# Optimization experiments

Hardware: AMD Instinct MI355X
Metric: run time of the kernel (lower is better)

## Reference

```python
import jax, jax.numpy as jnp
import numpy as np

C = 256
DR = 32  # C // reduction

def setup_inputs() -> dict:
    key = jax.random.key(0)
    ks = jax.random.split(key, 8)
    B, H, W = 8, 64, 64
    x = jax.random.normal(ks[0], (B, C, H, W), dtype=jnp.float32)
    # 1x1 conv weights stored as [out, in] matrices + biases
    sq = 1.0 / np.sqrt(C)
    Wq = jax.random.uniform(ks[1], (DR, C), minval=-sq, maxval=sq, dtype=jnp.float32)
    bq = jax.random.uniform(ks[2], (DR,), minval=-sq, maxval=sq, dtype=jnp.float32)
    Wk = jax.random.uniform(ks[3], (DR, C), minval=-sq, maxval=sq, dtype=jnp.float32)
    bk = jax.random.uniform(ks[4], (DR,), minval=-sq, maxval=sq, dtype=jnp.float32)
    Wv = jax.random.uniform(ks[5], (C, C), minval=-sq, maxval=sq, dtype=jnp.float32)
    bv = jax.random.uniform(ks[6], (C,), minval=-sq, maxval=sq, dtype=jnp.float32)
    gamma = jnp.zeros((1,), dtype=jnp.float32) + 0.5  # nonzero so output depends on attention
    return {"x": x, "Wq": Wq, "bq": bq, "Wk": Wk, "bk": bk, "Wv": Wv, "bv": bv, "gamma": gamma}

def reference(x, Wq, bq, Wk, bk, Wv, bv, gamma):
    B, Cc, H, W = x.shape
    N = H * W
    xf = x.reshape(B, Cc, N)                                   # [B,C,N]
    q = jnp.einsum('dc,bcn->bdn', Wq, xf) + bq[None, :, None]  # [B,DR,N]
    k = jnp.einsum('dc,bcn->bdn', Wk, xf) + bk[None, :, None]  # [B,DR,N]
    v = jnp.einsum('ec,bcn->ben', Wv, xf) + bv[None, :, None]  # [B,C,N]
    attn = jnp.einsum('bdi,bdj->bij', q, k)                    # [B,N,N]
    attn = jax.nn.softmax(attn, axis=-1)
    out = jnp.einsum('bcj,bij->bci', v, attn)                  # [B,C,N]
    out = out.reshape(B, Cc, H, W)
    return gamma * out + x
```

## Files before the change

### kernel.cpp

```cpp
#include <hip/hip_runtime.h>

#define LOG2E 1.44269504088896340736f

typedef short v8s __attribute__((ext_vector_type(8)));
typedef float v4f __attribute__((ext_vector_type(4)));
typedef unsigned int v2u __attribute__((ext_vector_type(2)));

__device__ __forceinline__ unsigned short f2bf(float f) {
  unsigned int u = __float_as_uint(f);
  u += 0x7fffu + ((u >> 16) & 1u);
  return (unsigned short)(u >> 16);
}

__device__ __forceinline__ unsigned int cvtpk(float lo, float hi) {
  unsigned int r;
  asm("v_cvt_pk_bf16_f32 %0, %1, %2" : "=v"(r) : "v"(lo), "v"(hi));
  return r;
}

#define MFMA16(a, b, c) __builtin_amdgcn_mfma_f32_16x16x32_bf16((a), (b), (c), 0, 0, 0)

static const int CCH = 256, NPIX = 4096;

__global__ void wconv_kernel(const float* __restrict__ Wq, const float* __restrict__ Wk,
                             const float* __restrict__ Wv, unsigned short* __restrict__ wqk,
                             unsigned short* __restrict__ wvb) {
  int idx = blockIdx.x * 256 + threadIdx.x;
  int tot = 64 * 256 + 256 * 256;
  for (int i = idx; i < tot; i += gridDim.x * 256) {
    if (i < 64 * 256) {
      float v = (i < 32 * 256) ? Wq[i] : Wk[i - 32 * 256];
      wqk[i] = f2bf(v);
    } else {
      wvb[i - 64 * 256] = f2bf(Wv[i - 64 * 256]);
    }
  }
}

__global__ void xpose_kernel(const float* __restrict__ x, unsigned short* __restrict__ xT) {
  __shared__ float tile[64][65];
  int bid = blockIdx.x;
  int b = bid >> 8;
  int c0 = ((bid >> 6) & 3) * 64;
  int n0 = (bid & 63) * 64;
  int t = threadIdx.x;
  const float* xp = x + ((size_t)b * CCH + c0) * NPIX + n0;
#pragma unroll
  for (int p = 0; p < 16; ++p) {
    int cc = p * 4 + (t >> 6);
    int nn = t & 63;
    tile[cc][nn] = xp[(size_t)cc * NPIX + nn];
  }
  __syncthreads();
  unsigned short* xo = xT + ((size_t)b * NPIX + n0) * CCH + c0;
#pragma unroll
  for (int p = 0; p < 8; ++p) {
    int nn = p * 8 + (t >> 5);
    int cc = (t & 31) * 2;
    unsigned int pk = (unsigned int)f2bf(tile[cc][nn]) |
                      ((unsigned int)f2bf(tile[cc + 1][nn]) << 16);
    *(unsigned int*)(xo + (size_t)nn * CCH + cc) = pk;
  }
}

__global__ __launch_bounds__(256, 2) void qkproj_kernel(
    const unsigned short* __restrict__ xT, const unsigned short* __restrict__ wqk,
    const float* __restrict__ bq, const float* __restrict__ bk,
    unsigned short* __restrict__ qb, unsigned short* __restrict__ kb) {
  int bid = blockIdx.x;
  int b = bid >> 6;
  int n0 = (bid & 63) * 64;
  int w = threadIdx.x >> 6, lane = threadIdx.x & 63, g = lane >> 4, li = lane & 15;
  int nrow = n0 + 16 * w;
  v4f acc[4];
#pragma unroll
  for (int dt = 0; dt < 4; ++dt) acc[dt] = (v4f){0.f, 0.f, 0.f, 0.f};
#pragma unroll
  for (int ks = 0; ks < 8; ++ks) {
    v8s a = *(const v8s*)(xT + ((size_t)(b * NPIX + nrow + li)) * CCH + ks * 32 + g * 8);
#pragma unroll
    for (int dt = 0; dt < 4; ++dt) {
      v8s bf = *(const v8s*)(wqk + (dt * 16 + li) * 256 + ks * 32 + g * 8);
      acc[dt] = MFMA16(a, bf, acc[dt]);
    }
  }
#pragma unroll
  for (int dt = 0; dt < 4; ++dt) {
    int d = (dt & 1) * 16 + li;
    float bias = (dt < 2) ? bq[d] : bk[d];
    unsigned short* op = (dt < 2) ? qb : kb;
#pragma unroll
    for (int r = 0; r < 4; ++r) {
      int n = nrow + 4 * g + r;
      op[((size_t)(b * NPIX + n)) * 32 + d] = f2bf(acc[dt][r] + bias);
    }
  }
}

__global__ __launch_bounds__(256, 2) void vproj_kernel(
    const unsigned short* __restrict__ xT, const unsigned short* __restrict__ wvb,
    const float* __restrict__ bv, unsigned short* __restrict__ vb) {
  int bid = blockIdx.x;
  int b = bid >> 6;
  int n0 = (bid & 63) * 64;
  int w = threadIdx.x >> 6, lane = threadIdx.x & 63, g = lane >> 4, li = lane & 15;
  v4f acc[4][4];
#pragma unroll
  for (int ct = 0; ct < 4; ++ct)
#pragma unroll
    for (int nt = 0; nt < 4; ++nt) acc[ct][nt] = (v4f){0.f, 0.f, 0.f, 0.f};
#pragma unroll
  for (int ks = 0; ks < 8; ++ks) {
    v8s xf[4];
#pragma unroll
    for (int nt = 0; nt < 4; ++nt)
      xf[nt] = *(const v8s*)(xT + ((size_t)(b * NPIX + n0 + nt * 16 + li)) * CCH + ks * 32 + g * 8);
#pragma unroll
    for (int ct = 0; ct < 4; ++ct) {
      v8s wf = *(const v8s*)(wvb + (w * 64 + ct * 16 + li) * 256 + ks * 32 + g * 8);
#pragma unroll
      for (int nt = 0; nt < 4; ++nt) acc[ct][nt] = MFMA16(wf, xf[nt], acc[ct][nt]);
    }
  }
#pragma unroll
  for (int ct = 0; ct < 4; ++ct)
#pragma unroll
    for (int r = 0; r < 4; ++r) {
      int c = w * 64 + ct * 16 + 4 * g + r;
      float bias = bv[c];
#pragma unroll
      for (int nt = 0; nt < 4; ++nt) {
        int n = n0 + nt * 16 + li;
        vb[((size_t)(b * CCH + c)) * NPIX + n] = f2bf(acc[ct][nt][r] + bias);
      }
    }
}

#define PSWZ(il, jl) (((il) * 64 + (jl)) ^ (((il) & 7) << 3))
__global__ __launch_bounds__(512, 4) void attn_kernel(
    const unsigned short* __restrict__ qb, const unsigned short* __restrict__ kb,
    const unsigned short* __restrict__ vb, const float* __restrict__ x,
    const float* __restrict__ gamma, float* __restrict__ out) {
  __shared__ __align__(16) unsigned short pbuf[2][64 * 64];
  __shared__ float fbuf[2][64];
  __shared__ float lbuf[64];
  int bx = blockIdx.x;
  int wg = (bx & 7) * 64 + (bx >> 3);
  int b = wg >> 6, it = wg & 63;
  int i0 = it * 64;
  int w = threadIdx.x >> 6, lane = threadIdx.x & 63, g = lane >> 4, li = lane & 15;
  bool prod = (w < 4);

  float mraw = -1e30f, ml2 = -1.44e30f, ls = 0.f;
  v4f acc[2][4];
#pragma unroll
  for (int ct = 0; ct < 2; ++ct)
#pragma unroll
    for (int itl = 0; itl < 4; ++itl) acc[ct][itl] = (v4f){0.f, 0.f, 0.f, 0.f};
  const v4f vzero = {0.f, 0.f, 0.f, 0.f};

  const unsigned short* vb0 = vb + ((size_t)(b * CCH + w * 32 + li)) * NPIX + g * 8;
  const unsigned short* vbc[2];
#pragma unroll
  for (int ct = 0; ct < 2; ++ct) vbc[ct] = vb0 + (size_t)ct * 16 * NPIX;

  const unsigned short* kbase = kb + ((size_t)b * NPIX + li) * 32 + g * 8;
  v8s qf = {0, 0, 0, 0, 0, 0, 0, 0};
  v8s kf[4];
  if (prod) {
    qf = *(const v8s*)(qb + ((size_t)(b * NPIX + i0 + w * 16 + li)) * 32 + g * 8);
#pragma unroll
    for (int jt = 0; jt < 4; ++jt) kf[jt] = *(const v8s*)(kbase + (size_t)(jt * 16) * 32);
  }

  for (int jc = 0; jc < 64; ++jc) {
    int j0 = jc * 64, bsel = jc & 1;
    v8s vf[2][2];
#pragma unroll
    for (int ct = 0; ct < 2; ++ct)
#pragma unroll
      for (int sl = 0; sl < 2; ++sl)
        vf[ct][sl] = *(const v8s*)(vbc[ct] + j0 + sl * 32);
    if (prod) {
      __builtin_amdgcn_s_setprio(1);
      v4f s[4];
#pragma unroll
      for (int jt = 0; jt < 4; ++jt) s[jt] = MFMA16(kf[jt], qf, vzero);
      int jn = (jc < 63) ? j0 + 64 : j0;
#pragma unroll
      for (int jt = 0; jt < 4; ++jt)
        kf[jt] = *(const v8s*)(kbase + (size_t)(jn + jt * 16) * 32);
      float t0 = fmaxf(fmaxf(s[0][0], s[0][1]), fmaxf(s[0][2], s[0][3]));
      float t1 = fmaxf(fmaxf(s[1][0], s[1][1]), fmaxf(s[1][2], s[1][3]));
      float t2 = fmaxf(fmaxf(s[2][0], s[2][1]), fmaxf(s[2][2], s[2][3]));
      float t3 = fmaxf(fmaxf(s[3][0], s[3][1]), fmaxf(s[3][2], s[3][3]));
      float pmax = fmaxf(fmaxf(t0, t1), fmaxf(t2, t3));
      pmax = fmaxf(pmax, __shfl_xor(pmax, 16, 64));
      pmax = fmaxf(pmax, __shfl_xor(pmax, 32, 64));
      bool upd = pmax > mraw + 8.f;
      float nml2 = upd ? pmax * LOG2E : ml2;
      float fsc = __builtin_amdgcn_exp2f(ml2 - nml2);
      if (upd) { mraw = pmax; ml2 = nml2; }
      int il = w * 16 + li;
      float rs = 0.f;
#pragma unroll
      for (int jt = 0; jt < 4; ++jt) {
        float p0 = __builtin_amdgcn_exp2f(fmaf(s[jt][0], LOG2E, -nml2));
        float p1 = __builtin_amdgcn_exp2f(fmaf(s[jt][1], LOG2E, -nml2));
        float p2 = __builtin_amdgcn_exp2f(fmaf(s[jt][2], LOG2E, -nml2));
        float p3 = __builtin_amdgcn_exp2f(fmaf(s[jt][3], LOG2E, -nml2));
        rs += (p0 + p1) + (p2 + p3);
        v2u pk;
        pk.x = cvtpk(p0, p1);
        pk.y = cvtpk(p2, p3);
        *(v2u*)(&pbuf[bsel][PSWZ(il, jt * 16 + 4 * g)]) = pk;
      }
      rs += __shfl_xor(rs, 16, 64);
      rs += __shfl_xor(rs, 32, 64);
      ls = ls * fsc + rs;
      if (g == 0) fbuf[bsel][il] = fsc;
      asm volatile("s_waitcnt lgkmcnt(0)" ::: "memory");
      __builtin_amdgcn_s_setprio(0);
    }
    __builtin_amdgcn_s_barrier();
    asm volatile("" ::: "memory");
    float fv[4];
#pragma unroll
    for (int itl = 0; itl < 4; ++itl) fv[itl] = fbuf[bsel][itl * 16 + li];
    int anyr = (fv[0] != 1.f) | (fv[1] != 1.f) | (fv[2] != 1.f) | (fv[3] != 1.f);
    if (__any(anyr)) {
#pragma unroll
      for (int itl = 0; itl < 4; ++itl)
#pragma unroll
        for (int ct = 0; ct < 2; ++ct) acc[ct][itl] = acc[ct][itl] * fv[itl];
    }
#pragma unroll
    for (int itl = 0; itl < 4; ++itl) {
      v8s pf[2];
#pragma unroll
      for (int sl = 0; sl < 2; ++sl)
        pf[sl] = *(const v8s*)(&pbuf[bsel][PSWZ(itl * 16 + li, sl * 32 + g * 8)]);
#pragma unroll
      for (int ct = 0; ct < 2; ++ct)
#pragma unroll
        for (int sl = 0; sl < 2; ++sl) acc[ct][itl] = MFMA16(vf[ct][sl], pf[sl], acc[ct][itl]);
    }
  }
  if (prod && g == 0) lbuf[w * 16 + li] = ls;
  __syncthreads();
  float gm = gamma[0];
#pragma unroll
  for (int itl = 0; itl < 4; ++itl) {
    float inv = gm / lbuf[itl * 16 + li];
#pragma unroll
    for (int ct = 0; ct < 2; ++ct)
#pragma unroll
      for (int r = 0; r < 4; ++r) {
        int c = w * 32 + ct * 16 + 4 * g + r;
        size_t idx = ((size_t)(b * CCH + c)) * NPIX + i0 + itl * 16 + li;
        out[idx] = acc[ct][itl][r] * inv + x[idx];
      }
  }
}

extern "C" void kernel_launch(void* const* d_in, const int* in_sizes, int n_in,
                              void* d_out, int out_size, void* d_ws, size_t ws_size,
                              hipStream_t stream) {
  const float* x = (const float*)d_in[0];
  const float* Wq = (const float*)d_in[1];
  const float* bq = (const float*)d_in[2];
  const float* Wk = (const float*)d_in[3];
  const float* bk = (const float*)d_in[4];
  const float* Wv = (const float*)d_in[5];
  const float* bv = (const float*)d_in[6];
  const float* gamma = (const float*)d_in[7];
  float* out = (float*)d_out;
  char* ws = (char*)d_ws;
  unsigned short* xT  = (unsigned short*)(ws);
  unsigned short* qb  = (unsigned short*)(ws + 16777216);
  unsigned short* kb  = (unsigned short*)(ws + 18874368);
  unsigned short* vb  = (unsigned short*)(ws + 20971520);
  unsigned short* wqk = (unsigned short*)(ws + 37748736);
  unsigned short* wvb = (unsigned short*)(ws + 37781504);

  wconv_kernel<<<80, 256, 0, stream>>>(Wq, Wk, Wv, wqk, wvb);
  xpose_kernel<<<2048, 256, 0, stream>>>(x, xT);
  qkproj_kernel<<<512, 256, 0, stream>>>(xT, wqk, bq, bk, qb, kb);
  vproj_kernel<<<512, 256, 0, stream>>>(xT, wvb, bv, vb);
  attn_kernel<<<512, 512, 0, stream>>>(qb, kb, vb, x, gamma, out);
}
```

Measured before the change: 276.6 us.

## Software-pipeline softmax one chunk ahead of PV MFMAs in attention kernel

Adds a prologue that computes the first chunk's softmax probabilities before the loop, so each iteration computes the next chunk's QK scores and softmax into the other buffer while running the PV MFMAs on the current one. This overlaps the producer waves' softmax with their own PV work, which should cut the serialized barrier-to-barrier critical path. The conditional rescale skip is dropped, so rescaling now always runs, and the K prefetch moves two chunks ahead. Register pressure goes up because the score and PV state are live at the same time.

```diff
diff --git a/kernel.cpp b/kernel.cpp
--- a/kernel.cpp
+++ b/kernel.cpp
@@ -137,6 +137,52 @@
 }
 
 #define PSWZ(il, jl) (((il) * 64 + (jl)) ^ (((il) & 7) << 3))
+
+#define SOFTMAX_PUBLISH(PB)                                                    \
+  do {                                                                         \
+    float t0 = fmaxf(fmaxf(s[0][0], s[0][1]), fmaxf(s[0][2], s[0][3]));        \
+    float t1 = fmaxf(fmaxf(s[1][0], s[1][1]), fmaxf(s[1][2], s[1][3]));        \
+    float t2 = fmaxf(fmaxf(s[2][0], s[2][1]), fmaxf(s[2][2], s[2][3]));        \
+    float t3 = fmaxf(fmaxf(s[3][0], s[3][1]), fmaxf(s[3][2], s[3][3]));        \
+    float pmax = fmaxf(fmaxf(t0, t1), fmaxf(t2, t3));                          \
+    pmax = fmaxf(pmax, __shfl_xor(pmax, 16, 64));                              \
+    pmax = fmaxf(pmax, __shfl_xor(pmax, 32, 64));                              \
+    bool upd = pmax > mraw + 8.f;                                              \
+    float nml2 = upd ? pmax * LOG2E : ml2;                                     \
+    float fsc = __builtin_amdgcn_exp2f(ml2 - nml2);                            \
+    if (upd) { mraw = pmax; ml2 = nml2; }                                      \
+    float rs = 0.f;                                                            \
+    _Pragma("unroll")                                                          \
+    for (int jt = 0; jt < 4; ++jt) {                                           \
+      float p0 = __builtin_amdgcn_exp2f(fmaf(s[jt][0], LOG2E, -nml2));         \
+      float p1 = __builtin_amdgcn_exp2f(fmaf(s[jt][1], LOG2E, -nml2));         \
+      float p2 = __builtin_amdgcn_exp2f(fmaf(s[jt][2], LOG2E, -nml2));         \
+      float p3 = __builtin_amdgcn_exp2f(fmaf(s[jt][3], LOG2E, -nml2));         \
+      rs += (p0 + p1) + (p2 + p3);                                             \
+      v2u pk;                                                                  \
+      pk.x = cvtpk(p0, p1);                                                    \
+      pk.y = cvtpk(p2, p3);                                                    \
+      *(v2u*)(&pbuf[PB][PSWZ(il, jt * 16 + 4 * g)]) = pk;                      \
+    }                                                                          \
+    rs += __shfl_xor(rs, 16, 64);                                              \
+    rs += __shfl_xor(rs, 32, 64);                                              \
+    ls = ls * fsc + rs;                                                        \
+    if (g == 0) fbuf[PB][il] = fsc;                                            \
+  } while (0)
+
+#define PV_BLOCK                                                               \
+  do {                                                                         \
+    _Pragma("unroll")                                                          \
+    for (int itl = 0; itl < 4; ++itl) {                                        \
+      v8s pf0 = *(const v8s*)(&pbuf[bsel][PSWZ(itl * 16 + li, g * 8)]);        \
+      v8s pf1 = *(const v8s*)(&pbuf[bsel][PSWZ(itl * 16 + li, 32 + g * 8)]);   \
+      acc[0][itl] = MFMA16(vf[0][0], pf0, acc[0][itl]);                        \
+      acc[0][itl] = MFMA16(vf[0][1], pf1, acc[0][itl]);                        \
+      acc[1][itl] = MFMA16(vf[1][0], pf0, acc[1][itl]);                        \
+      acc[1][itl] = MFMA16(vf[1][1], pf1, acc[1][itl]);                        \
+    }                                                                          \
+  } while (0)
+
 __global__ __launch_bounds__(512, 4) void attn_kernel(
     const unsigned short* __restrict__ qb, const unsigned short* __restrict__ kb,
     const unsigned short* __restrict__ vb, const float* __restrict__ x,
@@ -150,6 +196,7 @@
   int i0 = it * 64;
   int w = threadIdx.x >> 6, lane = threadIdx.x & 63, g = lane >> 4, li = lane & 15;
   bool prod = (w < 4);
+  int il = w * 16 + li;
 
   float mraw = -1e30f, ml2 = -1.44e30f, ls = 0.f;
   v4f acc[2][4];
@@ -167,86 +214,58 @@
   const unsigned short* kbase = kb + ((size_t)b * NPIX + li) * 32 + g * 8;
   v8s qf = {0, 0, 0, 0, 0, 0, 0, 0};
   v8s kf[4];
+
   if (prod) {
     qf = *(const v8s*)(qb + ((size_t)(b * NPIX + i0 + w * 16 + li)) * 32 + g * 8);
 #pragma unroll
     for (int jt = 0; jt < 4; ++jt) kf[jt] = *(const v8s*)(kbase + (size_t)(jt * 16) * 32);
-  }
+    v4f s[4];
+#pragma unroll
+    for (int jt = 0; jt < 4; ++jt) s[jt] = MFMA16(kf[jt], qf, vzero);
+#pragma unroll
+    for (int jt = 0; jt < 4; ++jt)
+      kf[jt] = *(const v8s*)(kbase + (size_t)(64 + jt * 16) * 32);
+    SOFTMAX_PUBLISH(0);
+    asm volatile("s_waitcnt lgkmcnt(0)" ::: "memory");
+  }
+  __builtin_amdgcn_s_barrier();
+  asm volatile("" ::: "memory");
 
   for (int jc = 0; jc < 64; ++jc) {
-    int j0 = jc * 64, bsel = jc & 1;
+    int j0 = jc * 64, bsel = jc & 1, nb = bsel ^ 1;
     v8s vf[2][2];
 #pragma unroll
     for (int ct = 0; ct < 2; ++ct)
 #pragma unroll
       for (int sl = 0; sl < 2; ++sl)
         vf[ct][sl] = *(const v8s*)(vbc[ct] + j0 + sl * 32);
-    if (prod) {
+    float fv[4];
+#pragma unroll
+    for (int itl = 0; itl < 4; ++itl) fv[itl] = fbuf[bsel][itl * 16 + li];
+#pragma unroll
+    for (int itl = 0; itl < 4; ++itl)
+#pragma unroll
+      for (int ct = 0; ct < 2; ++ct) acc[ct][itl] = acc[ct][itl] * fv[itl];
+    if (prod && jc < 63) {
       __builtin_amdgcn_s_setprio(1);
       v4f s[4];
 #pragma unroll
       for (int jt = 0; jt < 4; ++jt) s[jt] = MFMA16(kf[jt], qf, vzero);
-      int jn = (jc < 63) ? j0 + 64 : j0;
+      int jn = (jc < 62) ? (jc + 2) * 64 : 4032;
 #pragma unroll
       for (int jt = 0; jt < 4; ++jt)
         kf[jt] = *(const v8s*)(kbase + (size_t)(jn + jt * 16) * 32);
-      float t0 = fmaxf(fmaxf(s[0][0], s[0][1]), fmaxf(s[0][2], s[0][3]));
-      float t1 = fmaxf(fmaxf(s[1][0], s[1][1]), fmaxf(s[1][2], s[1][3]));
-      float t2 = fmaxf(fmaxf(s[2][0], s[2][1]), fmaxf(s[2][2], s[2][3]));
-      float t3 = fmaxf(fmaxf(s[3][0], s[3][1]), fmaxf(s[3][2], s[3][3]));
-      float pmax = fmaxf(fmaxf(t0, t1), fmaxf(t2, t3));
-      pmax = fmaxf(pmax, __shfl_xor(pmax, 16, 64));
-      pmax = fmaxf(pmax, __shfl_xor(pmax, 32, 64));
-      bool upd = pmax > mraw + 8.f;
-      float nml2 = upd ? pmax * LOG2E : ml2;
-      float fsc = __builtin_amdgcn_exp2f(ml2 - nml2);
-      if (upd) { mraw = pmax; ml2 = nml2; }
-      int il = w * 16 + li;
-      float rs = 0.f;
-#pragma unroll
-      for (int jt = 0; jt < 4; ++jt) {
-        float p0 = __builtin_amdgcn_exp2f(fmaf(s[jt][0], LOG2E, -nml2));
-        float p1 = __builtin_amdgcn_exp2f(fmaf(s[jt][1], LOG2E, -nml2));
-        float p2 = __builtin_amdgcn_exp2f(fmaf(s[jt][2], LOG2E, -nml2));
-        float p3 = __builtin_amdgcn_exp2f(fmaf(s[jt][3], LOG2E, -nml2));
-        rs += (p0 + p1) + (p2 + p3);
-        v2u pk;
-        pk.x = cvtpk(p0, p1);
-        pk.y = cvtpk(p2, p3);
-        *(v2u*)(&pbuf[bsel][PSWZ(il, jt * 16 + 4 * g)]) = pk;
-      }
-      rs += __shfl_xor(rs, 16, 64);
-      rs += __shfl_xor(rs, 32, 64);
-      ls = ls * fsc + rs;
-      if (g == 0) fbuf[bsel][il] = fsc;
+      SOFTMAX_PUBLISH(nb);
+      PV_BLOCK;
       asm volatile("s_waitcnt lgkmcnt(0)" ::: "memory");
       __builtin_amdgcn_s_setprio(0);
+    } else {
+      PV_BLOCK;
     }
     __builtin_amdgcn_s_barrier();
     asm volatile("" ::: "memory");
-    float fv[4];
-#pragma unroll
-    for (int itl = 0; itl < 4; ++itl) fv[itl] = fbuf[bsel][itl * 16 + li];
-    int anyr = (fv[0] != 1.f) | (fv[1] != 1.f) | (fv[2] != 1.f) | (fv[3] != 1.f);
-    if (__any(anyr)) {
-#pragma unroll
-      for (int itl = 0; itl < 4; ++itl)
-#pragma unroll
-        for (int ct = 0; ct < 2; ++ct) acc[ct][itl] = acc[ct][itl] * fv[itl];
-    }
-#pragma unroll
-    for (int itl = 0; itl < 4; ++itl) {
-      v8s pf[2];
-#pragma unroll
-      for (int sl = 0; sl < 2; ++sl)
-        pf[sl] = *(const v8s*)(&pbuf[bsel][PSWZ(itl * 16 + li, sl * 32 + g * 8)]);
-#pragma unroll
-      for (int ct = 0; ct < 2; ++ct)
-#pragma unroll
-        for (int sl = 0; sl < 2; ++sl) acc[ct][itl] = MFMA16(vf[ct][sl], pf[sl], acc[ct][itl]);
-    }
-  }
-  if (prod && g == 0) lbuf[w * 16 + li] = ls;
+  }
+  if (prod && g == 0) lbuf[il] = ls;
   __syncthreads();
   float gm = gamma[0];
 #pragma unroll
```

Measured after the change: 280.4 us. About the same (+1.4%).

## Fuse transpose and projections; split attention over key chunks with combine pass

Applied to the files above, without the earlier changes.

Merges the transpose, QK projection and V projection into one prep kernel that stages the bf16 transposed x tile in shared memory, so the xT round trip through global memory is gone. The attention kernel is templated to split the key dimension into JQ chunks, chosen from the workspace size. Each chunk writes unnormalized bf16 partial outputs plus max and sum, and a new combine kernel merges them with log-sum-exp weights and adds the residual. The split raises the grid from 512 to up to 2048 blocks to fill more CUs, at the cost of extra partial-output traffic, an extra launch, and a bf16 rounding of the partials.

```diff
diff --git a/kernel.cpp b/kernel.cpp
--- a/kernel.cpp
+++ b/kernel.cpp
@@ -10,6 +10,10 @@
   unsigned int u = __float_as_uint(f);
   u += 0x7fffu + ((u >> 16) & 1u);
   return (unsigned short)(u >> 16);
+}
+
+__device__ __forceinline__ float bf2f(unsigned short u) {
+  return __uint_as_float((unsigned int)u << 16);
 }
 
 __device__ __forceinline__ unsigned int cvtpk(float lo, float hi) {
@@ -37,119 +41,121 @@
   }
 }
 
-__global__ void xpose_kernel(const float* __restrict__ x, unsigned short* __restrict__ xT) {
+__global__ __launch_bounds__(256, 2) void prep_kernel(
+    const float* __restrict__ x, const unsigned short* __restrict__ wqk,
+    const unsigned short* __restrict__ wvb, const float* __restrict__ bq,
+    const float* __restrict__ bk, const float* __restrict__ bv,
+    unsigned short* __restrict__ qb, unsigned short* __restrict__ kb,
+    unsigned short* __restrict__ vb) {
   __shared__ float tile[64][65];
-  int bid = blockIdx.x;
-  int b = bid >> 8;
-  int c0 = ((bid >> 6) & 3) * 64;
-  int n0 = (bid & 63) * 64;
-  int t = threadIdx.x;
-  const float* xp = x + ((size_t)b * CCH + c0) * NPIX + n0;
-#pragma unroll
-  for (int p = 0; p < 16; ++p) {
-    int cc = p * 4 + (t >> 6);
-    int nn = t & 63;
-    tile[cc][nn] = xp[(size_t)cc * NPIX + nn];
-  }
-  __syncthreads();
-  unsigned short* xo = xT + ((size_t)b * NPIX + n0) * CCH + c0;
-#pragma unroll
-  for (int p = 0; p < 8; ++p) {
-    int nn = p * 8 + (t >> 5);
-    int cc = (t & 31) * 2;
-    unsigned int pk = (unsigned int)f2bf(tile[cc][nn]) |
-                      ((unsigned int)f2bf(tile[cc + 1][nn]) << 16);
-    *(unsigned int*)(xo + (size_t)nn * CCH + cc) = pk;
-  }
-}
-
-__global__ __launch_bounds__(256, 2) void qkproj_kernel(
-    const unsigned short* __restrict__ xT, const unsigned short* __restrict__ wqk,
-    const float* __restrict__ bq, const float* __restrict__ bk,
-    unsigned short* __restrict__ qb, unsigned short* __restrict__ kb) {
+  __shared__ unsigned short xl[64][264];
   int bid = blockIdx.x;
   int b = bid >> 6;
   int n0 = (bid & 63) * 64;
-  int w = threadIdx.x >> 6, lane = threadIdx.x & 63, g = lane >> 4, li = lane & 15;
-  int nrow = n0 + 16 * w;
-  v4f acc[4];
-#pragma unroll
-  for (int dt = 0; dt < 4; ++dt) acc[dt] = (v4f){0.f, 0.f, 0.f, 0.f};
-#pragma unroll
-  for (int ks = 0; ks < 8; ++ks) {
-    v8s a = *(const v8s*)(xT + ((size_t)(b * NPIX + nrow + li)) * CCH + ks * 32 + g * 8);
+  int t = threadIdx.x;
+#pragma unroll
+  for (int s = 0; s < 4; ++s) {
+    int c0 = s * 64;
+    const float* xp = x + ((size_t)b * CCH + c0) * NPIX + n0;
+#pragma unroll
+    for (int p = 0; p < 4; ++p) {
+      int cc = p * 16 + (t >> 4);
+      int nn = (t & 15) * 4;
+      float4 v = *(const float4*)(xp + (size_t)cc * NPIX + nn);
+      tile[cc][nn] = v.x; tile[cc][nn + 1] = v.y;
+      tile[cc][nn + 2] = v.z; tile[cc][nn + 3] = v.w;
+    }
+    __syncthreads();
+#pragma unroll
+    for (int p = 0; p < 8; ++p) {
+      int nn = p * 8 + (t >> 5);
+      int cc = (t & 31) * 2;
+      unsigned int pk = (unsigned int)f2bf(tile[cc][nn]) |
+                        ((unsigned int)f2bf(tile[cc + 1][nn]) << 16);
+      *(unsigned int*)(&xl[nn][c0 + cc]) = pk;
+    }
+    __syncthreads();
+  }
+  int w = t >> 6, lane = t & 63, g = lane >> 4, li = lane & 15;
+  {
+    v4f acc[4];
+#pragma unroll
+    for (int dt = 0; dt < 4; ++dt) acc[dt] = (v4f){0.f, 0.f, 0.f, 0.f};
+#pragma unroll
+    for (int ks = 0; ks < 8; ++ks) {
+      v8s a = *(const v8s*)(&xl[16 * w + li][ks * 32 + g * 8]);
+#pragma unroll
+      for (int dt = 0; dt < 4; ++dt) {
+        v8s bf = *(const v8s*)(wqk + (dt * 16 + li) * 256 + ks * 32 + g * 8);
+        acc[dt] = MFMA16(a, bf, acc[dt]);
+      }
+    }
 #pragma unroll
     for (int dt = 0; dt < 4; ++dt) {
-      v8s bf = *(const v8s*)(wqk + (dt * 16 + li) * 256 + ks * 32 + g * 8);
-      acc[dt] = MFMA16(a, bf, acc[dt]);
-    }
-  }
-#pragma unroll
-  for (int dt = 0; dt < 4; ++dt) {
-    int d = (dt & 1) * 16 + li;
-    float bias = (dt < 2) ? bq[d] : bk[d];
-    unsigned short* op = (dt < 2) ? qb : kb;
-#pragma unroll
-    for (int r = 0; r < 4; ++r) {
-      int n = nrow + 4 * g + r;
-      op[((size_t)(b * NPIX + n)) * 32 + d] = f2bf(acc[dt][r] + bias);
-    }
-  }
-}
-
-__global__ __launch_bounds__(256, 2) void vproj_kernel(
-    const unsigned short* __restrict__ xT, const unsigned short* __restrict__ wvb,
-    const float* __restrict__ bv, unsigned short* __restrict__ vb) {
-  int bid = blockIdx.x;
-  int b = bid >> 6;
-  int n0 = (bid & 63) * 64;
-  int w = threadIdx.x >> 6, lane = threadIdx.x & 63, g = lane >> 4, li = lane & 15;
-  v4f acc[4][4];
-#pragma unroll
-  for (int ct = 0; ct < 4; ++ct)
-#pragma unroll
-    for (int nt = 0; nt < 4; ++nt) acc[ct][nt] = (v4f){0.f, 0.f, 0.f, 0.f};
-#pragma unroll
-  for (int ks = 0; ks < 8; ++ks) {
-    v8s xf[4];
-#pragma unroll
-    for (int nt = 0; nt < 4; ++nt)
-      xf[nt] = *(const v8s*)(xT + ((size_t)(b * NPIX + n0 + nt * 16 + li)) * CCH + ks * 32 + g * 8);
-#pragma unroll
-    for (int ct = 0; ct < 4; ++ct) {
-      v8s wf = *(const v8s*)(wvb + (w * 64 + ct * 16 + li) * 256 + ks * 32 + g * 8);
-#pragma unroll
-      for (int nt = 0; nt < 4; ++nt) acc[ct][nt] = MFMA16(wf, xf[nt], acc[ct][nt]);
-    }
-  }
-#pragma unroll
-  for (int ct = 0; ct < 4; ++ct)
-#pragma unroll
-    for (int r = 0; r < 4; ++r) {
-      int c = w * 64 + ct * 16 + 4 * g + r;
-      float bias = bv[c];
-#pragma unroll
-      for (int nt = 0; nt < 4; ++nt) {
-        int n = n0 + nt * 16 + li;
-        vb[((size_t)(b * CCH + c)) * NPIX + n] = f2bf(acc[ct][nt][r] + bias);
-      }
-    }
+      int d = (dt & 1) * 16 + li;
+      float bias = (dt < 2) ? bq[d] : bk[d];
+      unsigned short* op = (dt < 2) ? qb : kb;
+#pragma unroll
+      for (int r = 0; r < 4; ++r) {
+        int n = n0 + 16 * w + 4 * g + r;
+        op[((size_t)(b * NPIX + n)) * 32 + d] = f2bf(acc[dt][r] + bias);
+      }
+    }
+  }
+  {
+    v4f acc[4][4];
+#pragma unroll
+    for (int ct = 0; ct < 4; ++ct)
+#pragma unroll
+      for (int nt = 0; nt < 4; ++nt) acc[ct][nt] = (v4f){0.f, 0.f, 0.f, 0.f};
+#pragma unroll
+    for (int ks = 0; ks < 8; ++ks) {
+      v8s xf[4];
+#pragma unroll
+      for (int nt = 0; nt < 4; ++nt)
+        xf[nt] = *(const v8s*)(&xl[nt * 16 + li][ks * 32 + g * 8]);
+#pragma unroll
+      for (int ct = 0; ct < 4; ++ct) {
+        v8s wf = *(const v8s*)(wvb + (w * 64 + ct * 16 + li) * 256 + ks * 32 + g * 8);
+#pragma unroll
+        for (int nt = 0; nt < 4; ++nt) acc[ct][nt] = MFMA16(wf, xf[nt], acc[ct][nt]);
+      }
+    }
+#pragma unroll
+    for (int ct = 0; ct < 4; ++ct)
+#pragma unroll
+      for (int r = 0; r < 4; ++r) {
+        int c = w * 64 + ct * 16 + 4 * g + r;
+        float bias = bv[c];
+#pragma unroll
+        for (int nt = 0; nt < 4; ++nt) {
+          int n = n0 + nt * 16 + li;
+          vb[((size_t)(b * CCH + c)) * NPIX + n] = f2bf(acc[ct][nt][r] + bias);
+        }
+      }
+  }
 }
 
 #define PSWZ(il, jl) (((il) * 64 + (jl)) ^ (((il) & 7) << 3))
+template <int JQ>
 __global__ __launch_bounds__(512, 4) void attn_kernel(
     const unsigned short* __restrict__ qb, const unsigned short* __restrict__ kb,
     const unsigned short* __restrict__ vb, const float* __restrict__ x,
-    const float* __restrict__ gamma, float* __restrict__ out) {
+    const float* __restrict__ gamma, float* __restrict__ out,
+    unsigned short* __restrict__ Opart, float* __restrict__ ml) {
   __shared__ __align__(16) unsigned short pbuf[2][64 * 64];
   __shared__ float fbuf[2][64];
   __shared__ float lbuf[64];
   int bx = blockIdx.x;
-  int wg = (bx & 7) * 64 + (bx >> 3);
+  int jq = bx >> 9;
+  int bxl = bx & 511;
+  int wg = (bxl & 7) * 64 + (bxl >> 3);
   int b = wg >> 6, it = wg & 63;
   int i0 = it * 64;
   int w = threadIdx.x >> 6, lane = threadIdx.x & 63, g = lane >> 4, li = lane & 15;
   bool prod = (w < 4);
+  const int NC = 64 / JQ;
+  int c0s = jq * NC, c0e = c0s + NC;
 
   float mraw = -1e30f, ml2 = -1.44e30f, ls = 0.f;
   v4f acc[2][4];
@@ -170,10 +176,11 @@
   if (prod) {
     qf = *(const v8s*)(qb + ((size_t)(b * NPIX + i0 + w * 16 + li)) * 32 + g * 8);
 #pragma unroll
-    for (int jt = 0; jt < 4; ++jt) kf[jt] = *(const v8s*)(kbase + (size_t)(jt * 16) * 32);
-  }
-
-  for (int jc = 0; jc < 64; ++jc) {
+    for (int jt = 0; jt < 4; ++jt)
+      kf[jt] = *(const v8s*)(kbase + (size_t)(c0s * 64 + jt * 16) * 32);
+  }
+
+  for (int jc = c0s; jc < c0e; ++jc) {
     int j0 = jc * 64, bsel = jc & 1;
     v8s vf[2][2];
 #pragma unroll
@@ -186,7 +193,7 @@
       v4f s[4];
 #pragma unroll
       for (int jt = 0; jt < 4; ++jt) s[jt] = MFMA16(kf[jt], qf, vzero);
-      int jn = (jc < 63) ? j0 + 64 : j0;
+      int jn = (jc < c0e - 1) ? j0 + 64 : j0;
 #pragma unroll
       for (int jt = 0; jt < 4; ++jt)
         kf[jt] = *(const v8s*)(kbase + (size_t)(jn + jt * 16) * 32);
@@ -246,20 +253,72 @@
         for (int sl = 0; sl < 2; ++sl) acc[ct][itl] = MFMA16(vf[ct][sl], pf[sl], acc[ct][itl]);
     }
   }
-  if (prod && g == 0) lbuf[w * 16 + li] = ls;
-  __syncthreads();
-  float gm = gamma[0];
-#pragma unroll
-  for (int itl = 0; itl < 4; ++itl) {
-    float inv = gm / lbuf[itl * 16 + li];
-#pragma unroll
-    for (int ct = 0; ct < 2; ++ct)
-#pragma unroll
-      for (int r = 0; r < 4; ++r) {
-        int c = w * 32 + ct * 16 + 4 * g + r;
-        size_t idx = ((size_t)(b * CCH + c)) * NPIX + i0 + itl * 16 + li;
-        out[idx] = acc[ct][itl][r] * inv + x[idx];
-      }
+  if constexpr (JQ == 1) {
+    if (prod && g == 0) lbuf[w * 16 + li] = ls;
+    __syncthreads();
+    float gm = gamma[0];
+#pragma unroll
+    for (int itl = 0; itl < 4; ++itl) {
+      float inv = gm / lbuf[itl * 16 + li];
+#pragma unroll
+      for (int ct = 0; ct < 2; ++ct)
+#pragma unroll
+        for (int r = 0; r < 4; ++r) {
+          int c = w * 32 + ct * 16 + 4 * g + r;
+          size_t idx = ((size_t)(b * CCH + c)) * NPIX + i0 + itl * 16 + li;
+          out[idx] = acc[ct][itl][r] * inv + x[idx];
+        }
+    }
+  } else {
+    if (prod && g == 0) {
+      int il = w * 16 + li;
+      ml[((size_t)(jq * 512 + wg)) * 128 + il] = ml2;
+      ml[((size_t)(jq * 512 + wg)) * 128 + 64 + il] = ls;
+    }
+    unsigned short* ob = Opart + ((size_t)(jq * 512 + wg)) * 256 * 64;
+#pragma unroll
+    for (int itl = 0; itl < 4; ++itl)
+#pragma unroll
+      for (int ct = 0; ct < 2; ++ct)
+#pragma unroll
+        for (int r = 0; r < 4; ++r) {
+          int c = w * 32 + ct * 16 + 4 * g + r;
+          ob[(size_t)c * 64 + itl * 16 + li] = f2bf(acc[ct][itl][r]);
+        }
+  }
+}
+
+template <int JQ>
+__global__ __launch_bounds__(256) void combine_kernel(
+    const unsigned short* __restrict__ Opart, const float* __restrict__ ml,
+    const float* __restrict__ x, const float* __restrict__ gamma,
+    float* __restrict__ out) {
+  int wg = blockIdx.x;
+  int t = threadIdx.x;
+  int il = t & 63, cq = t >> 6;
+  float m_g = -1e30f;
+#pragma unroll
+  for (int q = 0; q < JQ; ++q)
+    m_g = fmaxf(m_g, ml[((size_t)(q * 512 + wg)) * 128 + il]);
+  float w_q[JQ], l_g = 0.f;
+#pragma unroll
+  for (int q = 0; q < JQ; ++q) {
+    float wq = __builtin_amdgcn_exp2f(ml[((size_t)(q * 512 + wg)) * 128 + il] - m_g);
+    w_q[q] = wq;
+    l_g += wq * ml[((size_t)(q * 512 + wg)) * 128 + 64 + il];
+  }
+  int b = wg >> 6;
+  int i0 = (wg & 63) * 64;
+  float gm = gamma[0] / l_g;
+  const unsigned short* ob = Opart + (size_t)wg * 256 * 64;
+#pragma unroll 4
+  for (int c = cq * 64; c < cq * 64 + 64; ++c) {
+    float o = 0.f;
+#pragma unroll
+    for (int q = 0; q < JQ; ++q)
+      o += w_q[q] * bf2f(ob[(size_t)q * 512 * 256 * 64 + (size_t)c * 64 + il]);
+    size_t idx = ((size_t)(b * CCH + c)) * NPIX + i0 + il;
+    out[idx] = o * gm + x[idx];
   }
 }
 
@@ -276,16 +335,27 @@
   const float* gamma = (const float*)d_in[7];
   float* out = (float*)d_out;
   char* ws = (char*)d_ws;
-  unsigned short* xT  = (unsigned short*)(ws);
-  unsigned short* qb  = (unsigned short*)(ws + 16777216);
-  unsigned short* kb  = (unsigned short*)(ws + 18874368);
-  unsigned short* vb  = (unsigned short*)(ws + 20971520);
-  unsigned short* wqk = (unsigned short*)(ws + 37748736);
-  unsigned short* wvb = (unsigned short*)(ws + 37781504);
+  unsigned short* qb    = (unsigned short*)(ws);
+  unsigned short* kb    = (unsigned short*)(ws + 2097152);
+  unsigned short* vb    = (unsigned short*)(ws + 4194304);
+  unsigned short* wqk   = (unsigned short*)(ws + 20971520);
+  unsigned short* wvb   = (unsigned short*)(ws + 21004288);
+  float*          mlp   = (float*)(ws + 21135360);
+  unsigned short* Opart = (unsigned short*)(ws + 22282240);
+
+  int JQ = 1;
+  if (ws_size >= (size_t)22282240 + (size_t)4 * 16777216) JQ = 4;
+  else if (ws_size >= (size_t)22282240 + (size_t)2 * 16777216) JQ = 2;
 
   wconv_kernel<<<80, 256, 0, stream>>>(Wq, Wk, Wv, wqk, wvb);
-  xpose_kernel<<<2048, 256, 0, stream>>>(x, xT);
-  qkproj_kernel<<<512, 256, 0, stream>>>(xT, wqk, bq, bk, qb, kb);
-  vproj_kernel<<<512, 256, 0, stream>>>(xT, wvb, bv, vb);
-  attn_kernel<<<512, 512, 0, stream>>>(qb, kb, vb, x, gamma, out);
-}
+  prep_kernel<<<512, 256, 0, stream>>>(x, wqk, wvb, bq, bk, bv, qb, kb, vb);
+  if (JQ == 4) {
+    attn_kernel<4><<<2048, 512, 0, stream>>>(qb, kb, vb, x, gamma, out, Opart, mlp);
+    combine_kernel<4><<<512, 256, 0, stream>>>(Opart, mlp, x, gamma, out);
+  } else if (JQ == 2) {
+    attn_kernel<2><<<1024, 512, 0, stream>>>(qb, kb, vb, x, gamma, out, Opart, mlp);
+    combine_kernel<2><<<512, 256, 0, stream>>>(Opart, mlp, x, gamma, out);
+  } else {
+    attn_kernel<1><<<512, 512, 0, stream>>>(qb, kb, vb, x, gamma, out, Opart, mlp);
+  }
+}
```

After: 284.7 us. 2.9% more time.
